# Performance work log

Measured on AMD Instinct MI355X. Metric: run time of the kernel, lower is better.

Reference implementation:

```python
import jax, jax.numpy as jnp
import numpy as np

B, N, D, S, ITERS = 64, 2048, 256, 8, 3
SCALE = D ** -0.5
EPS_LN = 1e-5

def _ln(x, g, b):
    m = jnp.mean(x, axis=-1, keepdims=True)
    v = jnp.var(x, axis=-1, keepdims=True)
    return (x - m) / jnp.sqrt(v + EPS_LN) * g + b

def setup_inputs() -> dict:
    key = jax.random.key(0)
    ks = jax.random.split(key, 20)
    s = D ** -0.5
    f32 = jnp.float32
    return dict(
        x=jax.random.normal(ks[0], (B, N, D), f32),
        noise=jax.random.normal(ks[1], (B, S, D), f32),
        slots_mu=jax.random.normal(ks[2], (1, 1, D), f32),
        slots_sigma=jax.random.normal(ks[3], (1, 1, D), f32),
        Wq=jax.random.normal(ks[4], (D, D), f32) * s, bq=jnp.zeros((D,), f32),
        Wk=jax.random.normal(ks[5], (D, D), f32) * s, bk=jnp.zeros((D,), f32),
        Wv=jax.random.normal(ks[6], (D, D), f32) * s, bv=jnp.zeros((D,), f32),
        W_ih=jax.random.normal(ks[7], (3 * D, D), f32) * s, b_ih=jnp.zeros((3 * D,), f32),
        W_hh=jax.random.normal(ks[8], (3 * D, D), f32) * s, b_hh=jnp.zeros((3 * D,), f32),
        W1=jax.random.normal(ks[9], (D, D), f32) * s, b1=jnp.zeros((D,), f32),
        W2=jax.random.normal(ks[10], (D, D), f32) * s, b2=jnp.zeros((D,), f32),
        g_in=jnp.ones((D,), f32), be_in=jnp.zeros((D,), f32),
        g_sl=jnp.ones((D,), f32), be_sl=jnp.zeros((D,), f32),
        g_ff=jnp.ones((D,), f32), be_ff=jnp.zeros((D,), f32),
    )

def reference(x, noise, slots_mu, slots_sigma, Wq, bq, Wk, bk, Wv, bv,
              W_ih, b_ih, W_hh, b_hh, W1, b1, W2, b2,
              g_in, be_in, g_sl, be_sl, g_ff, be_ff):
    # slot init: mu + softplus(sigma) * noise  -> [B,S,D]
    slots = slots_mu + jax.nn.softplus(slots_sigma) * noise
    xn = _ln(x, g_in, be_in)
    k = xn @ Wk.T + bk  # [B,N,D]
    v = xn @ Wv.T + bv
    for _ in range(ITERS):
        prev = slots
        q = _ln(slots, g_sl, be_sl) @ Wq.T + bq  # [B,S,D]
        logits = jnp.einsum('bsd,bnd->bsn', q, k) * SCALE
        attn = jax.nn.softmax(logits, axis=-1) + 1e-8  # softmax over inputs, as in source
        attn = attn / jnp.sum(attn, axis=-1, keepdims=True)
        updates = jnp.einsum('bsn,bnd->bsd', attn, v)
        # GRUCell(input=updates, hidden=prev); torch gate order r,z,n
        gi = updates @ W_ih.T + b_ih
        gh = prev @ W_hh.T + b_hh
        ir, iz, i_n = jnp.split(gi, 3, axis=-1)
        hr, hz, h_n = jnp.split(gh, 3, axis=-1)
        r = jax.nn.sigmoid(ir + hr)
        z = jax.nn.sigmoid(iz + hz)
        n = jnp.tanh(i_n + r * h_n)
        slots = (1.0 - z) * n + z * prev
        # residual MLP
        h = jax.nn.relu(_ln(slots, g_ff, be_ff) @ W1.T + b1)
        slots = slots + (h @ W2.T + b2)
    return slots
```

## Files before the change

kernel.cpp:

```cpp
#include <hip/hip_runtime.h>
#include <cstddef>


#define BB 64
#define NN 2048
#define DD 256
#define NCH 16
#define CHK 128
#define NITER 3
#define XPITCH 264

typedef unsigned short u16;
typedef unsigned int u32;
typedef _Float16 h2 __attribute__((ext_vector_type(2)));
typedef _Float16 h4 __attribute__((ext_vector_type(4)));

#if defined(__has_builtin)
#if __has_builtin(__builtin_amdgcn_fdot2)
#define HAS_FDOT2 1
#endif
#endif

#ifdef HAS_FDOT2
#define FDOT2(a,b,c) __builtin_amdgcn_fdot2((a),(b),(c),false)
#else
#define FDOT2(a,b,c) fmaf((float)(a).y,(float)(b).y, fmaf((float)(a).x,(float)(b).x,(c)))
#endif

__device__ __forceinline__ h2 u2h2(u32 v){ union{u32 u; h2 h;} c; c.u=v; return c.h; }

__global__ __launch_bounds__(256) void kA(const float* __restrict__ noise, const float* __restrict__ mu,
                                          const float* __restrict__ sig, float* __restrict__ S,
                                          const float* __restrict__ Wq, const float* __restrict__ Wk,
                                          const float* __restrict__ bq, const float* __restrict__ Wih,
                                          const float* __restrict__ Wv, const float* __restrict__ bv,
                                          const float* __restrict__ bih,
                                          float* __restrict__ Wqk, float* __restrict__ bqk,
                                          float* __restrict__ Wihv, float* __restrict__ bihv){
  __shared__ float col[256];
  const int t = threadIdx.x;
  const int blk = blockIdx.x;
  if(blk < 256){
    col[t] = Wq[t*256 + blk];
    __syncthreads();
    float acc = 0.f;
    #pragma unroll 4
    for(int j=0;j<256;j++) acc += col[j]*Wk[j*256+t];
    Wqk[blk*256+t] = acc * 0.0625f;
  } else if(blk < 1024){
    int c = blk - 256;
    col[t] = Wih[c*256+t];
    __syncthreads();
    float acc = 0.f;
    #pragma unroll 4
    for(int j=0;j<256;j++) acc += col[j]*Wv[j*256+t];
    Wihv[(size_t)c*256+t] = acc;
  } else if(blk < 1536){
    int i = (blk-1024)*256 + t;
    float sg = sig[t];
    float sp = fmaxf(sg, 0.f) + log1pf(expf(-fabsf(sg)));
    S[i] = mu[t] + sp * noise[i];
  } else if(blk == 1536){
    float acc = 0.f;
    for(int j=0;j<256;j++) acc += bq[j]*Wk[j*256+t];
    bqk[t] = acc * 0.0625f;
  } else {
    for(int c=t;c<768;c+=256){
      float acc = 0.f;
      for(int j=0;j<256;j++) acc += Wih[c*256+j]*bv[j];
      bihv[c] = acc + bih[c];
    }
  }
}

__global__ __launch_bounds__(256) void kB(const float* __restrict__ Wihv, const float* __restrict__ Whh,
                                          const float* __restrict__ W1, const float* __restrict__ W2,
                                          float* __restrict__ WihvT, float* __restrict__ WhhT,
                                          float* __restrict__ W1T, float* __restrict__ W2T,
                                          const float* __restrict__ S0, const float* __restrict__ g_sl,
                                          const float* __restrict__ be_sl, const float* __restrict__ Wqk,
                                          const float* __restrict__ bqk, float* __restrict__ Qq){
  __shared__ float tile[64][65];
  __shared__ float lnA[8][256];
  const int blk = blockIdx.x, t = threadIdx.x;
  if(blk < 128){
    const float* src; float* dst; int R, C, tb;
    if(blk < 48){ src=Wihv; dst=WihvT; R=768; C=256; tb=blk; }
    else if(blk < 96){ src=Whh; dst=WhhT; R=768; C=256; tb=blk-48; }
    else if(blk < 112){ src=W1; dst=W1T; R=256; C=256; tb=blk-96; }
    else { src=W2; dst=W2T; R=256; C=256; tb=blk-112; }
    const int tilesC = C/64;
    const int r0 = (tb/tilesC)*64, c0 = (tb%tilesC)*64;
    const int x = t&63, y = t>>6;
    #pragma unroll
    for(int k=0;k<16;k++) tile[y*16+k][x] = src[(size_t)(r0+y*16+k)*C + c0+x];
    __syncthreads();
    #pragma unroll
    for(int k=0;k<16;k++) dst[(size_t)(c0+y*16+k)*R + r0+x] = tile[x][y*16+k];
    return;
  }
  const int w = t>>6, l = t&63;
  const int r0 = (blk-128)*8;
  #pragma unroll
  for(int rr=0; rr<2; rr++){
    int r = w*2 + rr;
    float4 v = *(const float4*)(S0 + (size_t)(r0+r)*256 + l*4);
    float s1 = v.x+v.y+v.z+v.w;
    float s2 = v.x*v.x+v.y*v.y+v.z*v.z+v.w*v.w;
    #pragma unroll
    for(int off=1; off<64; off<<=1){ s1 += __shfl_xor(s1,off); s2 += __shfl_xor(s2,off); }
    float m = s1*(1.f/256.f);
    float var = s2*(1.f/256.f) - m*m;
    float rs = rsqrtf(var + 1e-5f);
    float4 gg = *(const float4*)(g_sl + l*4);
    float4 bb = *(const float4*)(be_sl + l*4);
    float4 o;
    o.x=(v.x-m)*rs*gg.x+bb.x; o.y=(v.y-m)*rs*gg.y+bb.y;
    o.z=(v.z-m)*rs*gg.z+bb.z; o.w=(v.w-m)*rs*gg.w+bb.w;
    *(float4*)(&lnA[r][l*4]) = o;
  }
  __syncthreads();
  const int c4 = l*4;
  float acc[2][4] = {};
  #pragma unroll 2
  for(int k=0;k<256;k++){
    float4 wv = *(const float4*)(Wqk + (size_t)k*256 + c4);
    float a0 = lnA[2*w][k], a1 = lnA[2*w+1][k];
    acc[0][0]+=a0*wv.x; acc[0][1]+=a0*wv.y; acc[0][2]+=a0*wv.z; acc[0][3]+=a0*wv.w;
    acc[1][0]+=a1*wv.x; acc[1][1]+=a1*wv.y; acc[1][2]+=a1*wv.z; acc[1][3]+=a1*wv.w;
  }
  float4 bq4 = *(const float4*)(bqk + c4);
  #pragma unroll
  for(int rr=0; rr<2; rr++){
    float4 o;
    o.x=acc[rr][0]+bq4.x; o.y=acc[rr][1]+bq4.y; o.z=acc[rr][2]+bq4.z; o.w=acc[rr][3]+bq4.w;
    *(float4*)(Qq + (size_t)(r0+2*w+rr)*256 + c4) = o;
  }
}

__device__ __forceinline__ void attn_core(u16* xs, h2 (*qs)[128], float (*plT)[128],
                                          float* mS, float* lS,
                                          const float* __restrict__ Qq,
                                          float* __restrict__ mP, float* __restrict__ lP,
                                          float* __restrict__ aP, int b, int c, int t){
  const int w = t>>6, l = t&63;
  const int n = t & 127, sg = t >> 7;
  float lg[2]={0,0};
  {
    const u16* xr = xs + (size_t)n*XPITCH;
    #pragma unroll 4
    for(int d8=0; d8<32; ++d8){
      uint4 u = *(const uint4*)(xr + d8*8);
      h2 xa=u2h2(u.x), xb=u2h2(u.y), xc=u2h2(u.z), xd=u2h2(u.w);
      #pragma unroll
      for(int k=0;k<2;k++){
        const h2* qp = &qs[sg*2+k][d8*4];
        float acc = lg[k];
        acc = FDOT2(xa, qp[0], acc);
        acc = FDOT2(xb, qp[1], acc);
        acc = FDOT2(xc, qp[2], acc);
        acc = FDOT2(xd, qp[3], acc);
        lg[k] = acc;
      }
    }
    #pragma unroll
    for(int k=0;k<2;k++) plT[sg*2+k][n] = lg[k];
  }
  __syncthreads();
  {
    float mx = fmaxf(plT[w][l], plT[w][l+64]);
    #pragma unroll
    for(int off=1; off<64; off<<=1) mx = fmaxf(mx, __shfl_xor(mx, off));
    if(l==0) mS[w] = mx;
  }
  __syncthreads();
  #pragma unroll
  for(int k=0;k<2;k++) plT[sg*2+k][n] = __expf(lg[k] - mS[sg*2+k]);
  __syncthreads();
  {
    float sm = plT[w][l] + plT[w][l+64];
    #pragma unroll
    for(int off=1; off<64; off<<=1) sm += __shfl_xor(sm, off);
    if(l==0) lS[w] = sm;
  }
  __syncthreads();
  const size_t pb = (size_t)(b*NCH + c)*8;
  {
    float4 a4 = {0.f,0.f,0.f,0.f};
    const u16* xq = xs + 4*l;
    #pragma unroll 8
    for(int nn=0; nn<128; ++nn){
      uint2 u = *(const uint2*)(xq + (size_t)nn*XPITCH);
      h2 ha=u2h2(u.x), hb=u2h2(u.y);
      float p = plT[w][nn];
      a4.x += p*(float)ha.x; a4.y += p*(float)ha.y;
      a4.z += p*(float)hb.x; a4.w += p*(float)hb.y;
    }
    *(float4*)(aP + (pb + w)*256 + l*4) = a4;
  }
  if(t<8){ mP[pb+t] = mS[t]; lP[pb+t] = lS[t]; }
}

__global__ __launch_bounds__(512) void k_attn0(const float* __restrict__ x, const float* __restrict__ g_in,
                                               const float* __restrict__ be_in, u16* __restrict__ xn,
                                               const float* __restrict__ Qq,
                                               float* __restrict__ mP, float* __restrict__ lP,
                                               float* __restrict__ aP){
  __shared__ __align__(16) u16 xs[CHK*XPITCH];
  __shared__ h2 qs[8][128];
  __shared__ float plT[8][128];
  __shared__ float mS[8], lS[8];
  const int b = blockIdx.x, c = blockIdx.y, t = threadIdx.x;
  const int w = t>>6, l = t&63;
  {
    const size_t rowbase = (size_t)b*NN + (size_t)c*CHK;
    const float* xb = x + rowbase*DD;
    float4 gg = *(const float4*)(g_in + l*4);
    float4 bb = *(const float4*)(be_in + l*4);
    #pragma unroll 4
    for(int k=0;k<16;k++){
      int row = w + 8*k;
      float4 v = *(const float4*)(xb + (size_t)row*256 + l*4);
      float s1 = v.x+v.y+v.z+v.w;
      float s2 = v.x*v.x + v.y*v.y + v.z*v.z + v.w*v.w;
      #pragma unroll
      for(int off=1; off<64; off<<=1){ s1 += __shfl_xor(s1,off); s2 += __shfl_xor(s2,off); }
      float m = s1*(1.f/256.f);
      float var = s2*(1.f/256.f) - m*m;
      float rs = rsqrtf(var + 1e-5f);
      union { h4 h; uint2 u2v; } pk;
      pk.h[0] = (_Float16)((v.x-m)*rs*gg.x + bb.x);
      pk.h[1] = (_Float16)((v.y-m)*rs*gg.y + bb.y);
      pk.h[2] = (_Float16)((v.z-m)*rs*gg.z + bb.z);
      pk.h[3] = (_Float16)((v.w-m)*rs*gg.w + bb.w);
      *(uint2*)(xs + (size_t)row*XPITCH + l*4) = pk.u2v;
      *(uint2*)(xn + (rowbase+row)*DD + l*4) = pk.u2v;
    }
  }
  for(int i=t; i<1024; i+=512){
    int s = i>>7, p = i&127;
    float a = Qq[b*2048 + s*256 + 2*p];
    float bq = Qq[b*2048 + s*256 + 2*p + 1];
    h2 hv; hv.x = (_Float16)a; hv.y = (_Float16)bq;
    qs[s][p] = hv;
  }
  __syncthreads();
  attn_core(xs, qs, plT, mS, lS, Qq, mP, lP, aP, b, c, t);
}

__global__ __launch_bounds__(512) void k_attnN(const u16* __restrict__ xn, const float* __restrict__ Qq,
                                               float* __restrict__ mP, float* __restrict__ lP,
                                               float* __restrict__ aP){
  __shared__ __align__(16) u16 xs[CHK*XPITCH];
  __shared__ h2 qs[8][128];
  __shared__ float plT[8][128];
  __shared__ float mS[8], lS[8];
  const int b = blockIdx.x, c = blockIdx.y, t = threadIdx.x;
  {
    const uint4* xg4 = (const uint4*)(xn + ((size_t)b*NN + (size_t)c*CHK)*DD);
    #pragma unroll
    for(int k=0;k<8;k++){
      int idx = t + 512*k;
      int n = idx>>5, j = idx&31;
      *(uint4*)(xs + (size_t)n*XPITCH + j*8) = xg4[idx];
    }
  }
  for(int i=t; i<1024; i+=512){
    int s = i>>7, p = i&127;
    float a = Qq[b*2048 + s*256 + 2*p];
    float bq = Qq[b*2048 + s*256 + 2*p + 1];
    h2 hv; hv.x = (_Float16)a; hv.y = (_Float16)bq;
    qs[s][p] = hv;
  }
  __syncthreads();
  attn_core(xs, qs, plT, mS, lS, Qq, mP, lP, aP, b, c, t);
}

union PostU {
  float Gt[2][4][768];
  struct { float Row[4][256]; float Ht[4][256]; float Lq[4][256]; } m;
};

__global__ __launch_bounds__(512) void k_post(const float* __restrict__ mP, const float* __restrict__ lP,
                                              const float* __restrict__ aP, const float* __restrict__ WihvT,
                                              const float* __restrict__ bihv, const float* __restrict__ WhhT,
                                              const float* __restrict__ bhh, const float* __restrict__ Sc,
                                              const float* __restrict__ g_ff, const float* __restrict__ be_ff,
                                              const float* __restrict__ W1T, const float* __restrict__ b1,
                                              const float* __restrict__ W2T, const float* __restrict__ b2,
                                              const float* __restrict__ g_sl, const float* __restrict__ be_sl,
                                              const float* __restrict__ Wqk, const float* __restrict__ bqk,
                                              float* __restrict__ Sout, float* __restrict__ Qq, int writeQ){
  __shared__ float Ut[4][256];
  __shared__ float Sp[4][256];
  __shared__ float Hp[2][4][256];
  __shared__ PostU uu;
  __shared__ float red2[4][2];
  const int t = threadIdx.x;
  const int r0 = blockIdx.x*4;
  const int b = r0>>3;
  const int w = t>>6, l = t&63;
  const int c = t&255, hh = t>>8;

  #pragma unroll
  for(int k=0;k<2;k++){
    int idx = t + 512*k;
    int r = idx>>8, cc = idx&255;
    int rr = r0 + r, ss = rr&7;
    const float* mpb = mP + b*(NCH*8) + ss;
    const float* lpb = lP + b*(NCH*8) + ss;
    float M = -1e30f;
    #pragma unroll
    for(int c8=0;c8<NCH;c8++) M = fmaxf(M, mpb[c8*8]);
    float wc[NCH]; float L = 0.f;
    #pragma unroll
    for(int c8=0;c8<NCH;c8++){ wc[c8] = __expf(mpb[c8*8] - M); L += lpb[c8*8]*wc[c8]; }
    float inv = 1.f/L;
    size_t base = ((size_t)b*(NCH*8) + ss)*256 + cc;
    float u = 0.f;
    #pragma unroll
    for(int c8=0;c8<NCH;c8++) u += wc[c8]*aP[base + (size_t)c8*2048];
    Ut[r][cc] = u*inv;
    Sp[r][cc] = Sc[(size_t)rr*256 + cc];
  }
  __syncthreads();

  if(t < 384){
    const int mat = t/192, q4 = (t - mat*192)*4;
    const float* WT = mat ? WhhT : WihvT;
    const float* bb2 = mat ? bhh : bihv;
    const float (*A)[256] = mat ? Sp : Ut;
    float4 bias4 = *(const float4*)(bb2 + q4);
    float4 ac0 = bias4, ac1 = bias4, ac2 = bias4, ac3 = bias4;
    const float* wp = WT + q4;
    #pragma unroll 4
    for(int d=0; d<256; ++d){
      float4 wv = *(const float4*)(wp + (size_t)d*768);
      float a0=A[0][d], a1=A[1][d], a2=A[2][d], a3=A[3][d];
      ac0.x += a0*wv.x; ac0.y += a0*wv.y; ac0.z += a0*wv.z; ac0.w += a0*wv.w;
      ac1.x += a1*wv.x; ac1.y += a1*wv.y; ac1.z += a1*wv.z; ac1.w += a1*wv.w;
      ac2.x += a2*wv.x; ac2.y += a2*wv.y; ac2.z += a2*wv.z; ac2.w += a2*wv.w;
      ac3.x += a3*wv.x; ac3.y += a3*wv.y; ac3.z += a3*wv.z; ac3.w += a3*wv.w;
    }
    *(float4*)(&uu.Gt[mat][0][q4]) = ac0;
    *(float4*)(&uu.Gt[mat][1][q4]) = ac1;
    *(float4*)(&uu.Gt[mat][2][q4]) = ac2;
    *(float4*)(&uu.Gt[mat][3][q4]) = ac3;
  }
  __syncthreads();

  #pragma unroll
  for(int k=0;k<2;k++){
    int idx = t + 512*k;
    int r = idx>>8, cc = idx&255;
    float gir = uu.Gt[0][r][cc], giz = uu.Gt[0][r][256+cc], gin = uu.Gt[0][r][512+cc];
    float ghr = uu.Gt[1][r][cc], ghz = uu.Gt[1][r][256+cc], ghn = uu.Gt[1][r][512+cc];
    float rr2 = 1.f/(1.f + __expf(-(gir+ghr)));
    float zz = 1.f/(1.f + __expf(-(giz+ghz)));
    float nn = tanhf(gin + rr2*ghn);
    Ut[r][cc] = (1.f-zz)*nn + zz*Sp[r][cc];
  }
  __syncthreads();

  if(w < 4){
    float s1=0.f, s2=0.f;
    #pragma unroll
    for(int k2=0;k2<4;k2++){ float v = Ut[w][l + 64*k2]; s1 += v; s2 += v*v; }
    #pragma unroll
    for(int off=1; off<64; off<<=1){ s1 += __shfl_xor(s1,off); s2 += __shfl_xor(s2,off); }
    if(l==0){
      float m = s1*(1.f/256.f);
      float var = s2*(1.f/256.f) - m*m;
      red2[w][0] = m; red2[w][1] = rsqrtf(var + 1e-5f);
    }
  }
  __syncthreads();
  #pragma unroll
  for(int k=0;k<2;k++){
    int idx = t + 512*k;
    int r = idx>>8, cc = idx&255;
    uu.m.Row[r][cc] = (Ut[r][cc]-red2[r][0])*red2[r][1]*g_ff[cc] + be_ff[cc];
  }
  __syncthreads();

  {
    const float* w1 = W1T + (size_t)hh*128*256 + c;
    float a0 = hh ? 0.f : b1[c], a1=a0, a2=a0, a3=a0;
    const int dB = hh*128;
    #pragma unroll 8
    for(int d=0; d<128; ++d){
      float wv = w1[(size_t)d*256];
      a0 += uu.m.Row[0][dB+d]*wv;
      a1 += uu.m.Row[1][dB+d]*wv;
      a2 += uu.m.Row[2][dB+d]*wv;
      a3 += uu.m.Row[3][dB+d]*wv;
    }
    Hp[hh][0][c]=a0; Hp[hh][1][c]=a1; Hp[hh][2][c]=a2; Hp[hh][3][c]=a3;
  }
  __syncthreads();
  #pragma unroll
  for(int k=0;k<2;k++){
    int idx = t + 512*k;
    int r = idx>>8, cc = idx&255;
    uu.m.Ht[r][cc] = fmaxf(Hp[0][r][cc]+Hp[1][r][cc], 0.f);
  }
  __syncthreads();

  {
    const float* w2 = W2T + (size_t)hh*128*256 + c;
    float a0 = hh ? 0.f : b2[c], a1=a0, a2=a0, a3=a0;
    const int dB = hh*128;
    #pragma unroll 8
    for(int d=0; d<128; ++d){
      float wv = w2[(size_t)d*256];
      a0 += uu.m.Ht[0][dB+d]*wv;
      a1 += uu.m.Ht[1][dB+d]*wv;
      a2 += uu.m.Ht[2][dB+d]*wv;
      a3 += uu.m.Ht[3][dB+d]*wv;
    }
    Hp[hh][0][c]=a0; Hp[hh][1][c]=a1; Hp[hh][2][c]=a2; Hp[hh][3][c]=a3;
  }
  __syncthreads();
  if(t < 256){
    #pragma unroll
    for(int r=0;r<4;r++){
      float sn = Hp[0][r][c] + Hp[1][r][c] + Ut[r][c];
      Sout[(size_t)(r0+r)*256 + c] = sn;
      Ut[r][c] = sn;
    }
  }

  if(writeQ){
    __syncthreads();
    if(w < 4){
      float s1=0.f, s2=0.f;
      #pragma unroll
      for(int k2=0;k2<4;k2++){ float v = Ut[w][l + 64*k2]; s1 += v; s2 += v*v; }
      #pragma unroll
      for(int off=1; off<64; off<<=1){ s1 += __shfl_xor(s1,off); s2 += __shfl_xor(s2,off); }
      if(l==0){
        float m = s1*(1.f/256.f);
        float var = s2*(1.f/256.f) - m*m;
        red2[w][0] = m; red2[w][1] = rsqrtf(var + 1e-5f);
      }
    }
    __syncthreads();
    #pragma unroll
    for(int k=0;k<2;k++){
      int idx = t + 512*k;
      int r = idx>>8, cc = idx&255;
      uu.m.Lq[r][cc] = (Ut[r][cc]-red2[r][0])*red2[r][1]*g_sl[cc] + be_sl[cc];
    }
    __syncthreads();
    {
      const float* wq = Wqk + (size_t)hh*128*256 + c;
      float a0 = hh ? 0.f : bqk[c], a1=a0, a2=a0, a3=a0;
      const int dB = hh*128;
      #pragma unroll 8
      for(int d=0; d<128; ++d){
        float wv = wq[(size_t)d*256];
        a0 += uu.m.Lq[0][dB+d]*wv;
        a1 += uu.m.Lq[1][dB+d]*wv;
        a2 += uu.m.Lq[2][dB+d]*wv;
        a3 += uu.m.Lq[3][dB+d]*wv;
      }
      Hp[hh][0][c]=a0; Hp[hh][1][c]=a1; Hp[hh][2][c]=a2; Hp[hh][3][c]=a3;
    }
    __syncthreads();
    if(t < 256){
      #pragma unroll
      for(int r=0;r<4;r++)
        Qq[(size_t)(r0+r)*256 + c] = Hp[0][r][c] + Hp[1][r][c];
    }
  }
}

extern "C" void kernel_launch(void* const* d_in, const int* in_sizes, int n_in,
                              void* d_out, int out_size, void* d_ws, size_t ws_size,
                              hipStream_t stream){
  const float* x    = (const float*)d_in[0];
  const float* noise= (const float*)d_in[1];
  const float* mu   = (const float*)d_in[2];
  const float* sig  = (const float*)d_in[3];
  const float* Wq   = (const float*)d_in[4];
  const float* bq   = (const float*)d_in[5];
  const float* Wk   = (const float*)d_in[6];
  const float* Wv   = (const float*)d_in[8];
  const float* bv   = (const float*)d_in[9];
  const float* W_ih = (const float*)d_in[10];
  const float* b_ih = (const float*)d_in[11];
  const float* W_hh = (const float*)d_in[12];
  const float* b_hh = (const float*)d_in[13];
  const float* W1m  = (const float*)d_in[14];
  const float* b1v  = (const float*)d_in[15];
  const float* W2m  = (const float*)d_in[16];
  const float* b2v  = (const float*)d_in[17];
  const float* g_in = (const float*)d_in[18];
  const float* be_in= (const float*)d_in[19];
  const float* g_sl = (const float*)d_in[20];
  const float* be_sl= (const float*)d_in[21];
  const float* g_ff = (const float*)d_in[22];
  const float* be_ff= (const float*)d_in[23];

  char* p = (char*)d_ws;
  auto alloc = [&](size_t bytes)->char*{ char* q = p; p += (bytes + 255) & ~(size_t)255; return q; };
  u16*   xn    = (u16*)  alloc((size_t)BB*NN*DD*2);
  float* Wqk   = (float*)alloc(256*256*4);
  float* bqk   = (float*)alloc(256*4);
  float* Wihv  = (float*)alloc((size_t)768*256*4);
  float* WihvT = (float*)alloc((size_t)256*768*4);
  float* bihv  = (float*)alloc(768*4);
  float* WhhT  = (float*)alloc((size_t)256*768*4);
  float* W1T   = (float*)alloc(256*256*4);
  float* W2T   = (float*)alloc(256*256*4);
  float* S0    = (float*)alloc(512*256*4);
  float* S1    = (float*)alloc(512*256*4);
  float* Qq    = (float*)alloc(512*256*4);
  float* mP    = (float*)alloc(64*NCH*8*4);
  float* lP    = (float*)alloc(64*NCH*8*4);
  float* aP    = (float*)alloc((size_t)64*NCH*8*256*4);
  if((size_t)(p - (char*)d_ws) > ws_size) return;

  kA<<<1538, 256, 0, stream>>>(noise, mu, sig, S0, Wq, Wk, bq, W_ih, Wv, bv, b_ih,
                               Wqk, bqk, Wihv, bihv);
  kB<<<192, 256, 0, stream>>>(Wihv, W_hh, W1m, W2m, WihvT, WhhT, W1T, W2T,
                              S0, g_sl, be_sl, Wqk, bqk, Qq);

  float* Sin = S0;
  float* Sping[2] = { S1, S0 };
  for(int it=0; it<NITER; ++it){
    float* Sout = (it==NITER-1) ? (float*)d_out : Sping[it&1];
    if(it == 0)
      k_attn0<<<dim3(64, NCH), 512, 0, stream>>>(x, g_in, be_in, xn, Qq, mP, lP, aP);
    else
      k_attnN<<<dim3(64, NCH), 512, 0, stream>>>(xn, Qq, mP, lP, aP);
    k_post<<<128, 512, 0, stream>>>(mP, lP, aP, WihvT, bihv, WhhT, b_hh, Sin, g_ff, be_ff,
                                    W1T, b1v, W2T, b2v, g_sl, be_sl, Wqk, bqk,
                                    Sout, Qq, (it<NITER-1) ? 1 : 0);
    Sin = Sout;
  }
}
```

Measured before the change: 313.7 us.

## Halve attention chunk size, use wave-local softmax, store partials in fp16

```diff
diff --git a/kernel.cpp b/kernel.cpp
--- a/kernel.cpp
+++ b/kernel.cpp
@@ -5,8 +5,8 @@
 #define BB 64
 #define NN 2048
 #define DD 256
-#define NCH 16
-#define CHK 128
+#define NCH 32
+#define CHK 64
 #define NITER 3
 #define XPITCH 264
 
@@ -28,6 +28,7 @@
 #endif
 
 __device__ __forceinline__ h2 u2h2(u32 v){ union{u32 u; h2 h;} c; c.u=v; return c.h; }
+__device__ __forceinline__ float u16f(u16 v){ union{u16 u; _Float16 h;} c; c.u=v; return (float)c.h; }
 
 __global__ __launch_bounds__(256) void kA(const float* __restrict__ noise, const float* __restrict__ mu,
                                           const float* __restrict__ sig, float* __restrict__ S,
@@ -138,65 +139,51 @@
   }
 }
 
-__device__ __forceinline__ void attn_core(u16* xs, h2 (*qs)[128], float (*plT)[128],
+__device__ __forceinline__ void attn_core(const u16* xs, const h2 (*qs)[128], float (*plT)[64],
                                           float* mS, float* lS,
-                                          const float* __restrict__ Qq,
                                           float* __restrict__ mP, float* __restrict__ lP,
-                                          float* __restrict__ aP, int b, int c, int t){
+                                          u16* __restrict__ aPh, int b, int c, int t){
   const int w = t>>6, l = t&63;
-  const int n = t & 127, sg = t >> 7;
-  float lg[2]={0,0};
+  float lg = 0.f;
   {
-    const u16* xr = xs + (size_t)n*XPITCH;
+    const u16* xr = xs + (size_t)l*XPITCH;
     #pragma unroll 4
     for(int d8=0; d8<32; ++d8){
       uint4 u = *(const uint4*)(xr + d8*8);
       h2 xa=u2h2(u.x), xb=u2h2(u.y), xc=u2h2(u.z), xd=u2h2(u.w);
-      #pragma unroll
-      for(int k=0;k<2;k++){
-        const h2* qp = &qs[sg*2+k][d8*4];
-        float acc = lg[k];
-        acc = FDOT2(xa, qp[0], acc);
-        acc = FDOT2(xb, qp[1], acc);
-        acc = FDOT2(xc, qp[2], acc);
-        acc = FDOT2(xd, qp[3], acc);
-        lg[k] = acc;
-      }
-    }
-    #pragma unroll
-    for(int k=0;k<2;k++) plT[sg*2+k][n] = lg[k];
-  }
-  __syncthreads();
-  {
-    float mx = fmaxf(plT[w][l], plT[w][l+64]);
-    #pragma unroll
-    for(int off=1; off<64; off<<=1) mx = fmaxf(mx, __shfl_xor(mx, off));
-    if(l==0) mS[w] = mx;
-  }
-  __syncthreads();
-  #pragma unroll
-  for(int k=0;k<2;k++) plT[sg*2+k][n] = __expf(lg[k] - mS[sg*2+k]);
-  __syncthreads();
-  {
-    float sm = plT[w][l] + plT[w][l+64];
-    #pragma unroll
-    for(int off=1; off<64; off<<=1) sm += __shfl_xor(sm, off);
-    if(l==0) lS[w] = sm;
-  }
+      const h2* qp = &qs[w][d8*4];
+      lg = FDOT2(xa, qp[0], lg);
+      lg = FDOT2(xb, qp[1], lg);
+      lg = FDOT2(xc, qp[2], lg);
+      lg = FDOT2(xd, qp[3], lg);
+    }
+  }
+  float mx = lg;
+  #pragma unroll
+  for(int off=1; off<64; off<<=1) mx = fmaxf(mx, __shfl_xor(mx, off));
+  float p = __expf(lg - mx);
+  float sm = p;
+  #pragma unroll
+  for(int off=1; off<64; off<<=1) sm += __shfl_xor(sm, off);
+  plT[w][l] = p;
+  if(l==0){ mS[w] = mx; lS[w] = sm; }
   __syncthreads();
   const size_t pb = (size_t)(b*NCH + c)*8;
   {
     float4 a4 = {0.f,0.f,0.f,0.f};
     const u16* xq = xs + 4*l;
     #pragma unroll 8
-    for(int nn=0; nn<128; ++nn){
+    for(int nn=0; nn<64; ++nn){
       uint2 u = *(const uint2*)(xq + (size_t)nn*XPITCH);
       h2 ha=u2h2(u.x), hb=u2h2(u.y);
-      float p = plT[w][nn];
-      a4.x += p*(float)ha.x; a4.y += p*(float)ha.y;
-      a4.z += p*(float)hb.x; a4.w += p*(float)hb.y;
-    }
-    *(float4*)(aP + (pb + w)*256 + l*4) = a4;
+      float pp = plT[w][nn];
+      a4.x += pp*(float)ha.x; a4.y += pp*(float)ha.y;
+      a4.z += pp*(float)hb.x; a4.w += pp*(float)hb.y;
+    }
+    union { h4 h; uint2 u2v; } pk;
+    pk.h[0]=(_Float16)a4.x; pk.h[1]=(_Float16)a4.y;
+    pk.h[2]=(_Float16)a4.z; pk.h[3]=(_Float16)a4.w;
+    *(uint2*)(aPh + (pb + w)*256 + l*4) = pk.u2v;
   }
   if(t<8){ mP[pb+t] = mS[t]; lP[pb+t] = lS[t]; }
 }
@@ -205,10 +192,10 @@
                                                const float* __restrict__ be_in, u16* __restrict__ xn,
                                                const float* __restrict__ Qq,
                                                float* __restrict__ mP, float* __restrict__ lP,
-                                               float* __restrict__ aP){
+                                               u16* __restrict__ aPh){
   __shared__ __align__(16) u16 xs[CHK*XPITCH];
   __shared__ h2 qs[8][128];
-  __shared__ float plT[8][128];
+  __shared__ float plT[8][64];
   __shared__ float mS[8], lS[8];
   const int b = blockIdx.x, c = blockIdx.y, t = threadIdx.x;
   const int w = t>>6, l = t&63;
@@ -217,24 +204,31 @@
     const float* xb = x + rowbase*DD;
     float4 gg = *(const float4*)(g_in + l*4);
     float4 bb = *(const float4*)(be_in + l*4);
-    #pragma unroll 4
-    for(int k=0;k<16;k++){
-      int row = w + 8*k;
-      float4 v = *(const float4*)(xb + (size_t)row*256 + l*4);
-      float s1 = v.x+v.y+v.z+v.w;
-      float s2 = v.x*v.x + v.y*v.y + v.z*v.z + v.w*v.w;
+    #pragma unroll
+    for(int k=0;k<4;k++){
+      int r0 = w + 16*k, r1 = w + 16*k + 8;
+      float4 v0 = *(const float4*)(xb + (size_t)r0*256 + l*4);
+      float4 v1 = *(const float4*)(xb + (size_t)r1*256 + l*4);
+      float a1 = v0.x+v0.y+v0.z+v0.w;
+      float a2 = v0.x*v0.x + v0.y*v0.y + v0.z*v0.z + v0.w*v0.w;
+      float b1 = v1.x+v1.y+v1.z+v1.w;
+      float b2 = v1.x*v1.x + v1.y*v1.y + v1.z*v1.z + v1.w*v1.w;
       #pragma unroll
-      for(int off=1; off<64; off<<=1){ s1 += __shfl_xor(s1,off); s2 += __shfl_xor(s2,off); }
-      float m = s1*(1.f/256.f);
-      float var = s2*(1.f/256.f) - m*m;
-      float rs = rsqrtf(var + 1e-5f);
-      union { h4 h; uint2 u2v; } pk;
-      pk.h[0] = (_Float16)((v.x-m)*rs*gg.x + bb.x);
-      pk.h[1] = (_Float16)((v.y-m)*rs*gg.y + bb.y);
-      pk.h[2] = (_Float16)((v.z-m)*rs*gg.z + bb.z);
-      pk.h[3] = (_Float16)((v.w-m)*rs*gg.w + bb.w);
-      *(uint2*)(xs + (size_t)row*XPITCH + l*4) = pk.u2v;
-      *(uint2*)(xn + (rowbase+row)*DD + l*4) = pk.u2v;
+      for(int off=1; off<64; off<<=1){
+        a1 += __shfl_xor(a1,off); a2 += __shfl_xor(a2,off);
+        b1 += __shfl_xor(b1,off); b2 += __shfl_xor(b2,off);
+      }
+      float m0 = a1*(1.f/256.f), va0 = a2*(1.f/256.f) - m0*m0, rs0 = rsqrtf(va0 + 1e-5f);
+      float m1 = b1*(1.f/256.f), va1 = b2*(1.f/256.f) - m1*m1, rs1 = rsqrtf(va1 + 1e-5f);
+      union { h4 h; uint2 u2v; } p0, p1;
+      p0.h[0]=(_Float16)((v0.x-m0)*rs0*gg.x+bb.x); p0.h[1]=(_Float16)((v0.y-m0)*rs0*gg.y+bb.y);
+      p0.h[2]=(_Float16)((v0.z-m0)*rs0*gg.z+bb.z); p0.h[3]=(_Float16)((v0.w-m0)*rs0*gg.w+bb.w);
+      p1.h[0]=(_Float16)((v1.x-m1)*rs1*gg.x+bb.x); p1.h[1]=(_Float16)((v1.y-m1)*rs1*gg.y+bb.y);
+      p1.h[2]=(_Float16)((v1.z-m1)*rs1*gg.z+bb.z); p1.h[3]=(_Float16)((v1.w-m1)*rs1*gg.w+bb.w);
+      *(uint2*)(xs + (size_t)r0*XPITCH + l*4) = p0.u2v;
+      *(uint2*)(xs + (size_t)r1*XPITCH + l*4) = p1.u2v;
+      *(uint2*)(xn + (rowbase+r0)*DD + l*4) = p0.u2v;
+      *(uint2*)(xn + (rowbase+r1)*DD + l*4) = p1.u2v;
     }
   }
   for(int i=t; i<1024; i+=512){
@@ -245,21 +239,21 @@
     qs[s][p] = hv;
   }
   __syncthreads();
-  attn_core(xs, qs, plT, mS, lS, Qq, mP, lP, aP, b, c, t);
+  attn_core(xs, qs, plT, mS, lS, mP, lP, aPh, b, c, t);
 }
 
 __global__ __launch_bounds__(512) void k_attnN(const u16* __restrict__ xn, const float* __restrict__ Qq,
                                                float* __restrict__ mP, float* __restrict__ lP,
-                                               float* __restrict__ aP){
+                                               u16* __restrict__ aPh){
   __shared__ __align__(16) u16 xs[CHK*XPITCH];
   __shared__ h2 qs[8][128];
-  __shared__ float plT[8][128];
+  __shared__ float plT[8][64];
   __shared__ float mS[8], lS[8];
   const int b = blockIdx.x, c = blockIdx.y, t = threadIdx.x;
   {
     const uint4* xg4 = (const uint4*)(xn + ((size_t)b*NN + (size_t)c*CHK)*DD);
     #pragma unroll
-    for(int k=0;k<8;k++){
+    for(int k=0;k<4;k++){
       int idx = t + 512*k;
       int n = idx>>5, j = idx&31;
       *(uint4*)(xs + (size_t)n*XPITCH + j*8) = xg4[idx];
@@ -273,7 +267,7 @@
     qs[s][p] = hv;
   }
   __syncthreads();
-  attn_core(xs, qs, plT, mS, lS, Qq, mP, lP, aP, b, c, t);
+  attn_core(xs, qs, plT, mS, lS, mP, lP, aPh, b, c, t);
 }
 
 union PostU {
@@ -282,7 +276,7 @@
 };
 
 __global__ __launch_bounds__(512) void k_post(const float* __restrict__ mP, const float* __restrict__ lP,
-                                              const float* __restrict__ aP, const float* __restrict__ WihvT,
+                                              const u16* __restrict__ aPh, const float* __restrict__ WihvT,
                                               const float* __restrict__ bihv, const float* __restrict__ WhhT,
                                               const float* __restrict__ bhh, const float* __restrict__ Sc,
                                               const float* __restrict__ g_ff, const float* __restrict__ be_ff,
@@ -312,14 +306,15 @@
     float M = -1e30f;
     #pragma unroll
     for(int c8=0;c8<NCH;c8++) M = fmaxf(M, mpb[c8*8]);
-    float wc[NCH]; float L = 0.f;
+    float L = 0.f;
+    float wc[NCH];
     #pragma unroll
     for(int c8=0;c8<NCH;c8++){ wc[c8] = __expf(mpb[c8*8] - M); L += lpb[c8*8]*wc[c8]; }
     float inv = 1.f/L;
     size_t base = ((size_t)b*(NCH*8) + ss)*256 + cc;
     float u = 0.f;
     #pragma unroll
-    for(int c8=0;c8<NCH;c8++) u += wc[c8]*aP[base + (size_t)c8*2048];
+    for(int c8=0;c8<NCH;c8++) u += wc[c8]*u16f(aPh[base + (size_t)c8*2048]);
     Ut[r][cc] = u*inv;
     Sp[r][cc] = Sc[(size_t)rr*256 + cc];
   }
@@ -518,7 +513,7 @@
   float* Qq    = (float*)alloc(512*256*4);
   float* mP    = (float*)alloc(64*NCH*8*4);
   float* lP    = (float*)alloc(64*NCH*8*4);
-  float* aP    = (float*)alloc((size_t)64*NCH*8*256*4);
+  u16*   aPh   = (u16*)  alloc((size_t)64*NCH*8*256*2);
   if((size_t)(p - (char*)d_ws) > ws_size) return;
 
   kA<<<1538, 256, 0, stream>>>(noise, mu, sig, S0, Wq, Wk, bq, W_ih, Wv, bv, b_ih,
@@ -531,10 +526,10 @@
   for(int it=0; it<NITER; ++it){
     float* Sout = (it==NITER-1) ? (float*)d_out : Sping[it&1];
     if(it == 0)
-      k_attn0<<<dim3(64, NCH), 512, 0, stream>>>(x, g_in, be_in, xn, Qq, mP, lP, aP);
+      k_attn0<<<dim3(64, NCH), 512, 0, stream>>>(x, g_in, be_in, xn, Qq, mP, lP, aPh);
     else
-      k_attnN<<<dim3(64, NCH), 512, 0, stream>>>(xn, Qq, mP, lP, aP);
-    k_post<<<128, 512, 0, stream>>>(mP, lP, aP, WihvT, bihv, WhhT, b_hh, Sin, g_ff, be_ff,
+      k_attnN<<<dim3(64, NCH), 512, 0, stream>>>(xn, Qq, mP, lP, aPh);
+    k_post<<<128, 512, 0, stream>>>(mP, lP, aPh, WihvT, bihv, WhhT, b_hh, Sin, g_ff, be_ff,
                                     W1T, b1v, W2T, b2v, g_sl, be_sl, Wqk, bqk,
                                     Sout, Qq, (it<NITER-1) ? 1 : 0);
     Sin = Sout;
```

Result: no change. 311.9 us (-0.6%).
